# Kernel optimization log

Measured on AMD Instinct MI355X. Metric: run time of the kernel, lower is better.

## Reference

```python
import jax, jax.numpy as jnp
import numpy as np

N_NODES = 100000
N_EDGES = 3200000
NUM_FEATURES = 128
HIDDEN = 16


def _gcn_norm(edge_index, num_nodes):
    # Add self-loops and compute symmetric normalization D^{-1/2} (A+I) D^{-1/2}
    loops = jnp.arange(num_nodes, dtype=edge_index.dtype)
    row = jnp.concatenate([edge_index[0], loops])  # source j
    col = jnp.concatenate([edge_index[1], loops])  # target i
    ones = jnp.ones(row.shape[0], dtype=jnp.float32)
    deg = jax.ops.segment_sum(ones, col, num_segments=num_nodes)
    deg_inv_sqrt = jnp.where(deg > 0, jax.lax.rsqrt(deg), 0.0)
    norm = deg_inv_sqrt[row] * deg_inv_sqrt[col]  # [E + N]
    return row, col, norm


def _gcn_conv(x, row, col, norm, W, b, num_nodes):
    h = x @ W                                   # [N, out] linear first (PyG order)
    msg = h[row] * norm[:, None]                # gather + edge-wise scale
    out = jax.ops.segment_sum(msg, col, num_segments=num_nodes)  # scatter-add
    return out + b                              # bias after aggregation (PyG)


def setup_inputs() -> dict:
    key = jax.random.key(0)
    k1, k2, k3, k4, k5 = jax.random.split(key, 5)
    x = jax.random.normal(k1, (N_NODES, NUM_FEATURES), dtype=jnp.float32)
    edge_index = jax.random.randint(k2, (2, N_EDGES), 0, N_NODES, dtype=jnp.int64)
    # Glorot-style init for GCNConv linear weights
    W1 = jax.random.normal(k3, (NUM_FEATURES, HIDDEN), dtype=jnp.float32) / np.sqrt(NUM_FEATURES)
    b1 = jnp.zeros((HIDDEN,), dtype=jnp.float32)
    W2 = jax.random.normal(k4, (HIDDEN, 1), dtype=jnp.float32) / np.sqrt(HIDDEN)
    b2 = jnp.zeros((1,), dtype=jnp.float32)
    return {"x": x, "edge_index": edge_index, "W1": W1, "b1": b1, "W2": W2, "b2": b2}


def reference(x, edge_index, W1, b1, W2, b2):
    num_nodes = x.shape[0]
    row, col, norm = _gcn_norm(edge_index, num_nodes)  # shared by both layers
    h = _gcn_conv(x, row, col, norm, W1, b1, num_nodes)
    h = jax.nn.relu(h)
    out = _gcn_conv(h, row, col, norm, W2, b2, num_nodes)
    return out
```

## Files before the change

### kernel.cpp

```cpp
#include <hip/hip_runtime.h>
#include <hip/hip_fp16.h>


#define CB 8
#define CAP 9216
#define TILE 4096

__global__ void k_init_gcur(int* __restrict__ gcur, int nb) {
    int b = blockIdx.x * blockDim.x + threadIdx.x;
    if (b < nb) gcur[b] = b * CAP;
}

__global__ void __launch_bounds__(256) k_partition(
        const int* __restrict__ row, const int* __restrict__ col,
        int* __restrict__ gcur, int* __restrict__ ebuf, int e, int nb) {
    __shared__ int hist[512];
    __shared__ int gbase[512];
    const int base = blockIdx.x * TILE;
    for (int t = threadIdx.x; t < nb; t += 256) hist[t] = 0;
    __syncthreads();
#pragma unroll
    for (int k = 0; k < 16; ++k) {
        int i = base + (k << 8) + threadIdx.x;
        if (i < e) atomicAdd(&hist[col[i] >> CB], 1);
    }
    __syncthreads();
    for (int t = threadIdx.x; t < nb; t += 256) {
        int h = hist[t];
        gbase[t] = h ? atomicAdd(&gcur[t], h) : 0;
        hist[t] = 0;
    }
    __syncthreads();
#pragma unroll
    for (int k = 0; k < 16; ++k) {
        int i = base + (k << 8) + threadIdx.x;
        if (i < e) {
            int c = col[i], r = row[i];
            int b = c >> CB;
            int p = gbase[b] + atomicAdd(&hist[b], 1);
            if (p < (b + 1) * CAP)
                ebuf[p] = ((c & ((1 << CB) - 1)) << 17) | r;
        }
    }
}

__global__ void __launch_bounds__(256) k_bucket(
        const int* __restrict__ ebuf, const int* __restrict__ gcur,
        int* __restrict__ begA, int* __restrict__ endA, int* __restrict__ ssrc,
        float* __restrict__ dis, int n) {
    __shared__ int ev[CAP];
    __shared__ int hist[256];
    __shared__ int sc[256];
    const int b = blockIdx.x, t = threadIdx.x;
    const int base = b * CAP;
    const int cnt = gcur[b] - base;
    for (int j = t; j < cnt; j += 256) ev[j] = ebuf[base + j];
    hist[t] = 0;
    __syncthreads();
    for (int j = t; j < cnt; j += 256) atomicAdd(&hist[ev[j] >> 17], 1);
    __syncthreads();
    int v = hist[t];
    sc[t] = v;
    __syncthreads();
    for (int off = 1; off < 256; off <<= 1) {
        int add = (t >= off) ? sc[t - off] : 0;
        __syncthreads();
        sc[t] += add;
        __syncthreads();
    }
    int excl = sc[t] - v;
    int node = (b << CB) + t;
    if (node < n) {
        begA[node] = base + excl;
        endA[node] = base + excl + v;
        dis[node] = rsqrtf((float)(v + 1));
    }
    hist[t] = excl;
    __syncthreads();
    for (int j = t; j < cnt; j += 256) {
        int val = ev[j];
        int p = atomicAdd(&hist[val >> 17], 1);
        ssrc[base + p] = val & 0x1FFFF;
    }
}

__global__ void k_gemm1(const float* __restrict__ x, const float* __restrict__ W1,
                        const float* __restrict__ dis, __half* __restrict__ gh, int n) {
    __shared__ float wt[16 * 128];
    for (int t = threadIdx.x; t < 2048; t += blockDim.x) {
        int j = t >> 7, k = t & 127;
        wt[t] = W1[k * 16 + j];
    }
    __syncthreads();
    int r = blockIdx.x * blockDim.x + threadIdx.x;
    if (r >= n) return;
    const float4* x4 = (const float4*)(x + (size_t)r * 128);
    const float4* w4 = (const float4*)wt;
    float acc[16];
#pragma unroll
    for (int j = 0; j < 16; ++j) acc[j] = 0.f;
    for (int k4 = 0; k4 < 32; ++k4) {
        float4 vv = x4[k4];
#pragma unroll
        for (int j = 0; j < 16; ++j) {
            float4 w = w4[j * 32 + k4];
            acc[j] += vv.x * w.x + vv.y * w.y + vv.z * w.z + vv.w * w.w;
        }
    }
    float d = dis[r];
    __half2 hh[8];
#pragma unroll
    for (int j = 0; j < 8; ++j)
        hh[j] = __floats2half2_rn(d * acc[2 * j], d * acc[2 * j + 1]);
    uint4* o = (uint4*)(gh + (size_t)r * 16);
    const uint4* src = (const uint4*)hh;
    o[0] = src[0];
    o[1] = src[1];
}

__global__ void k_gather1(const int* __restrict__ begA, const int* __restrict__ endA,
                          const int* __restrict__ ssrc,
                          const __half2* __restrict__ g2, const float* __restrict__ dis,
                          const float* __restrict__ b1, const float* __restrict__ W2,
                          float* __restrict__ tbuf, int n) {
    int t = blockIdx.x * blockDim.x + threadIdx.x;
    if (t >= n * 8) return;
    int i = t >> 3, f2 = t & 7;
    float di = dis[i];
    int beg = begA[i], end = endA[i];
    float2 acc = __half22float2(g2[(size_t)i * 8 + f2]);
    for (int e = beg; e < end; ++e) {
        float2 v = __half22float2(g2[(size_t)ssrc[e] * 8 + f2]);
        acc.x += v.x;
        acc.y += v.y;
    }
    int f = f2 * 2;
    float u = fmaxf(di * acc.x + b1[f], 0.f) * W2[f]
            + fmaxf(di * acc.y + b1[f + 1], 0.f) * W2[f + 1];
#pragma unroll
    for (int m = 4; m >= 1; m >>= 1) u += __shfl_xor(u, m, 8);
    if (f2 == 0) tbuf[i] = di * u;
}

__global__ void k_gather2(const int* __restrict__ begA, const int* __restrict__ endA,
                          const int* __restrict__ ssrc,
                          const float* __restrict__ tbuf, const float* __restrict__ dis,
                          const float* __restrict__ b2, float* __restrict__ out, int n) {
    int t = blockIdx.x * blockDim.x + threadIdx.x;
    if (t >= n * 8) return;
    int i = t >> 3, l = t & 7;
    int beg = begA[i], end = endA[i];
    float acc = (l == 0) ? tbuf[i] : 0.f;
    for (int e = beg + l; e < end; e += 8) acc += tbuf[ssrc[e]];
#pragma unroll
    for (int m = 4; m >= 1; m >>= 1) acc += __shfl_xor(acc, m, 8);
    if (l == 0) out[i] = dis[i] * acc + b2[0];
}

extern "C" void kernel_launch(void* const* d_in, const int* in_sizes, int n_in,
                              void* d_out, int out_size, void* d_ws, size_t ws_size,
                              hipStream_t stream) {
    const float* x  = (const float*)d_in[0];
    const int*   ei = (const int*)d_in[1];
    const float* W1 = (const float*)d_in[2];
    const float* b1 = (const float*)d_in[3];
    const float* W2 = (const float*)d_in[4];
    const float* b2 = (const float*)d_in[5];
    float* out = (float*)d_out;

    const int N = in_sizes[0] / 128;
    const int E = in_sizes[1] / 2;
    const int* row = ei;
    const int* col = ei + E;
    const int NB = (N + 255) >> CB;
    const size_t PADE = (size_t)NB * CAP;

    size_t bigsz = PADE > (size_t)N * 8 ? PADE : (size_t)N * 8;
    int*    ebuf = (int*)d_ws;
    __half* gh   = (__half*)d_ws;
    int*    ssrc = (int*)d_ws + bigsz;
    float*  dis  = (float*)(ssrc + PADE);
    float*  tbuf = dis + N;
    int*    begA = (int*)(tbuf + N);
    int*    endA = begA + N;
    int*    gcur = endA + N;

    auto cdiv = [](int a, int b) { return (a + b - 1) / b; };

    k_init_gcur<<<cdiv(NB, 256),    256, 0, stream>>>(gcur, NB);
    k_partition<<<cdiv(E, TILE),    256, 0, stream>>>(row, col, gcur, ebuf, E, NB);
    k_bucket   <<<NB,               256, 0, stream>>>(ebuf, gcur, begA, endA, ssrc, dis, N);
    k_gemm1    <<<cdiv(N, 256),     256, 0, stream>>>(x, W1, dis, gh, N);
    k_gather1  <<<cdiv(N * 8, 256), 256, 0, stream>>>(begA, endA, ssrc, (const __half2*)gh,
                                                      dis, b1, W2, tbuf, N);
    k_gather2  <<<cdiv(N * 8, 256), 256, 0, stream>>>(begA, endA, ssrc, tbuf, dis, b2, out, N);
}
```

Baseline: 253.7 us.

## Stage partitioned edges in shared memory for coalesced bucket writes

Result: faster. 238.9 us (-5.8%).

```diff
diff --git a/kernel.cpp b/kernel.cpp
--- a/kernel.cpp
+++ b/kernel.cpp
@@ -11,36 +11,57 @@
     if (b < nb) gcur[b] = b * CAP;
 }
 
-__global__ void __launch_bounds__(256) k_partition(
+__global__ void __launch_bounds__(512) k_partition(
         const int* __restrict__ row, const int* __restrict__ col,
         int* __restrict__ gcur, int* __restrict__ ebuf, int e, int nb) {
     __shared__ int hist[512];
-    __shared__ int gbase[512];
+    __shared__ int lbase[512];
+    __shared__ int gdelta[512];
+    __shared__ int sval[TILE];
+    __shared__ unsigned short sbkt[TILE];
     const int base = blockIdx.x * TILE;
-    for (int t = threadIdx.x; t < nb; t += 256) hist[t] = 0;
-    __syncthreads();
-#pragma unroll
-    for (int k = 0; k < 16; ++k) {
-        int i = base + (k << 8) + threadIdx.x;
+    const int cnt = min(TILE, e - base);
+    const int t = threadIdx.x;
+    hist[t] = 0;
+    __syncthreads();
+#pragma unroll
+    for (int k = 0; k < TILE / 512; ++k) {
+        int i = base + (k << 9) + t;
         if (i < e) atomicAdd(&hist[col[i] >> CB], 1);
     }
     __syncthreads();
-    for (int t = threadIdx.x; t < nb; t += 256) {
-        int h = hist[t];
-        gbase[t] = h ? atomicAdd(&gcur[t], h) : 0;
-        hist[t] = 0;
-    }
-    __syncthreads();
-#pragma unroll
-    for (int k = 0; k < 16; ++k) {
-        int i = base + (k << 8) + threadIdx.x;
+    int v = hist[t];
+    lbase[t] = v;
+    __syncthreads();
+    for (int off = 1; off < 512; off <<= 1) {
+        int add = (t >= off) ? lbase[t - off] : 0;
+        __syncthreads();
+        lbase[t] += add;
+        __syncthreads();
+    }
+    int excl = lbase[t] - v;
+    __syncthreads();
+    lbase[t] = excl;
+    int gb = v ? atomicAdd(&gcur[t], v) : 0;
+    gdelta[t] = gb - excl;
+    hist[t] = excl;
+    __syncthreads();
+#pragma unroll
+    for (int k = 0; k < TILE / 512; ++k) {
+        int i = base + (k << 9) + t;
         if (i < e) {
             int c = col[i], r = row[i];
             int b = c >> CB;
-            int p = gbase[b] + atomicAdd(&hist[b], 1);
-            if (p < (b + 1) * CAP)
-                ebuf[p] = ((c & ((1 << CB) - 1)) << 17) | r;
+            int p = atomicAdd(&hist[b], 1);
+            sval[p] = ((c & ((1 << CB) - 1)) << 17) | r;
+            sbkt[p] = (unsigned short)b;
         }
+    }
+    __syncthreads();
+    for (int j = t; j < cnt; j += 512) {
+        int b = sbkt[j];
+        int p = gdelta[b] + j;
+        if (p < (b + 1) * CAP) ebuf[p] = sval[j];
     }
 }
 
@@ -48,16 +69,14 @@
         const int* __restrict__ ebuf, const int* __restrict__ gcur,
         int* __restrict__ begA, int* __restrict__ endA, int* __restrict__ ssrc,
         float* __restrict__ dis, int n) {
-    __shared__ int ev[CAP];
     __shared__ int hist[256];
     __shared__ int sc[256];
     const int b = blockIdx.x, t = threadIdx.x;
     const int base = b * CAP;
-    const int cnt = gcur[b] - base;
-    for (int j = t; j < cnt; j += 256) ev[j] = ebuf[base + j];
+    const int cnt = min(gcur[b] - base, CAP);
     hist[t] = 0;
     __syncthreads();
-    for (int j = t; j < cnt; j += 256) atomicAdd(&hist[ev[j] >> 17], 1);
+    for (int j = t; j < cnt; j += 256) atomicAdd(&hist[ebuf[base + j] >> 17], 1);
     __syncthreads();
     int v = hist[t];
     sc[t] = v;
@@ -78,7 +97,7 @@
     hist[t] = excl;
     __syncthreads();
     for (int j = t; j < cnt; j += 256) {
-        int val = ev[j];
+        int val = ebuf[base + j];
         int p = atomicAdd(&hist[val >> 17], 1);
         ssrc[base + p] = val & 0x1FFFF;
     }
@@ -188,7 +207,7 @@
     auto cdiv = [](int a, int b) { return (a + b - 1) / b; };
 
     k_init_gcur<<<cdiv(NB, 256),    256, 0, stream>>>(gcur, NB);
-    k_partition<<<cdiv(E, TILE),    256, 0, stream>>>(row, col, gcur, ebuf, E, NB);
+    k_partition<<<cdiv(E, TILE),    512, 0, stream>>>(row, col, gcur, ebuf, E, NB);
     k_bucket   <<<NB,               256, 0, stream>>>(ebuf, gcur, begA, endA, ssrc, dis, N);
     k_gemm1    <<<cdiv(N, 256),     256, 0, stream>>>(x, W1, dis, gh, N);
     k_gather1  <<<cdiv(N * 8, 256), 256, 0, stream>>>(begA, endA, ssrc, (const __half2*)gh,
```
